# Performance work log

Hardware: AMD Instinct MI355X
Metric: run time of the kernel (lower is better)

Reference implementation:

```python
import jax, jax.numpy as jnp
from jax import lax
import numpy as np

B, T, K = 128, 256, 600


def setup_inputs() -> dict:
    key = jax.random.key(0)
    k1, k2, k3, k4 = jax.random.split(key, 4)
    potentials = jax.random.normal(k1, (B, T, K), dtype=jnp.float32)
    transitions = jax.random.normal(k2, (K, K), dtype=jnp.float32) * 0.1
    tags = jax.random.randint(k3, (B, T), 0, K, dtype=jnp.int32)
    seq_len = jax.random.randint(k4, (B,), T // 2, T + 1, dtype=jnp.int32)
    return {"potentials": potentials, "transitions": transitions,
            "tags": tags, "seq_len": seq_len}


def _sequence_score(potentials, transitions, tags, mask):
    # unary (emission) scores: sum_t potentials[b, t, tags[b, t]] over valid t
    emit = jnp.take_along_axis(potentials, tags[..., None], axis=-1)[..., 0]  # [B,T]
    unary = jnp.sum(emit * mask, axis=1)
    # binary (transition) scores for valid consecutive pairs
    trans = transitions[tags[:, :-1], tags[:, 1:]]  # [B,T-1]
    binary = jnp.sum(trans * mask[:, 1:], axis=1)
    return unary + binary


def _log_norm(potentials, transitions, mask):
    # forward algorithm over time via scan; alpha: [B,K]
    def step(alpha, inp):
        emit_t, mask_t = inp  # [B,K], [B]
        scores = alpha[:, :, None] + transitions[None]      # [B,K,K]
        new = jax.nn.logsumexp(scores, axis=1) + emit_t     # [B,K]
        alpha = jnp.where(mask_t[:, None], new, alpha)
        return alpha, None

    alpha0 = potentials[:, 0]
    xs = (jnp.swapaxes(potentials[:, 1:], 0, 1),
          jnp.swapaxes(mask[:, 1:] > 0, 0, 1))
    alpha, _ = lax.scan(step, alpha0, xs)
    return jax.nn.logsumexp(alpha, axis=-1)  # [B]


def _viterbi(potentials, transitions, mask):
    idk = jnp.arange(K, dtype=jnp.int32)

    def step(alpha, inp):
        emit_t, mask_t = inp
        scores = alpha[:, :, None] + transitions[None]   # [B,K,K]
        bp = jnp.argmax(scores, axis=1).astype(jnp.int32)  # [B,K]
        new = jnp.max(scores, axis=1) + emit_t
        alpha = jnp.where(mask_t[:, None], new, alpha)
        bp = jnp.where(mask_t[:, None], bp, idk[None, :])  # identity past seq end
        return alpha, bp

    alpha0 = potentials[:, 0]
    xs = (jnp.swapaxes(potentials[:, 1:], 0, 1),
          jnp.swapaxes(mask[:, 1:] > 0, 0, 1))
    alpha, bps = lax.scan(step, alpha0, xs)  # bps: [T-1,B,K]
    last = jnp.argmax(alpha, axis=-1).astype(jnp.int32)  # [B]

    def back(tag, bp):
        prev = jnp.take_along_axis(bp, tag[:, None], axis=1)[:, 0]
        return prev, prev

    _, prevs = lax.scan(back, last, bps, reverse=True)  # [T-1,B]
    seq = jnp.concatenate([prevs, last[None]], axis=0)  # [T,B]
    seq = jnp.swapaxes(seq, 0, 1)                       # [B,T]
    return seq * mask.astype(jnp.int32)


def reference(potentials, transitions, tags, seq_len):
    mask = (jnp.arange(T)[None, :] < seq_len[:, None]).astype(potentials.dtype)  # [B,T]
    score = _sequence_score(potentials, transitions, tags, mask)
    log_norm = _log_norm(potentials, transitions, mask)
    log_likelihood = score - log_norm            # [B]
    crf_loss = -jnp.mean(log_likelihood)         # scalar, as in train_step
    decode_sequence = _viterbi(potentials, transitions, mask)  # [B,T]
    return crf_loss, decode_sequence
```

## Files before the change

### kernel.cpp

```cpp
#include <hip/hip_runtime.h>
#include <stdint.h>

#define CRF_B 128
#define CRF_T 256
#define CRF_K 600
#define FWD_NT 640
#define NWAVE 10
#define QW 152
#define QG 96
#define QSTR (QW - QG)
#define ESC 60.0f
#define INV7620 (1.0f/7620.0f)

#if __has_builtin(__builtin_amdgcn_sdot4)
#define DOT4(a,b,c) __builtin_amdgcn_sdot4((int)(a),(int)(b),(int)(c),false)
#else
__device__ __forceinline__ int DOT4(uint32_t a, uint32_t b, int c) {
    c += (int)(int8_t)(a)       * (int)(int8_t)(b);
    c += (int)(int8_t)(a >> 8)  * (int)(int8_t)(b >> 8);
    c += (int)(int8_t)(a >> 16) * (int)(int8_t)(b >> 16);
    c += (int)(int8_t)(a >> 24) * (int)(int8_t)(b >> 24);
    return c;
}
#endif

__device__ __forceinline__ uint32_t fmono(float x) {
    uint32_t k = __float_as_uint(x);
    return (k & 0x80000000u) ? ~k : (k | 0x80000000u);
}
__device__ __forceinline__ float funmono(uint32_t k) {
    return __uint_as_float((k & 0x80000000u) ? (k ^ 0x80000000u) : ~k);
}

__global__ __launch_bounds__(256) void prepE_kernel(const float* __restrict__ trans,
                                                    uint32_t* __restrict__ EqT)
{
    int idx = blockIdx.x * 256 + threadIdx.x;
    if (idx < QW * CRF_K) {
        int q = idx / CRF_K, j = idx % CRF_K;
        uint32_t w = 0;
        #pragma unroll
        for (int k = 0; k < 4; ++k) {
            int i = 4 * q + k;
            int b = 0;
            if (i < CRF_K) {
                b = __float2int_rn(ESC * __expf(trans[i * CRF_K + j]));
                b = min(127, max(0, b));
            }
            w |= ((uint32_t)(b & 0xff)) << (8 * k);
        }
        EqT[idx] = w;
    }
}

__global__ __launch_bounds__(64) void prep2_kernel(const float* __restrict__ trans,
                                                   float* __restrict__ rowmax,
                                                   float* __restrict__ rowmin)
{
    int r = blockIdx.x;
    int lane = threadIdx.x;
    float mx = -INFINITY, mn = INFINITY;
    for (int j = lane; j < CRF_K; j += 64) {
        float v = trans[r * CRF_K + j];
        mx = fmaxf(mx, v);
        mn = fminf(mn, v);
    }
    for (int o = 32; o; o >>= 1) {
        mx = fmaxf(mx, __shfl_down(mx, o));
        mn = fminf(mn, __shfl_down(mn, o));
    }
    if (lane == 0) { rowmax[r] = mx; rowmin[r] = mn; }
}

__global__ __launch_bounds__(64) void score_kernel(const float* __restrict__ pot,
                                                   const float* __restrict__ trans,
                                                   const int* __restrict__ tags,
                                                   const int* __restrict__ seq_len,
                                                   float* __restrict__ scoreArr)
{
    int b = blockIdx.x;
    int lane = threadIdx.x;
    int L = seq_len[b];
    float s = 0.f;
    for (int t = lane; t < CRF_T; t += 64) {
        if (t < L) {
            int tg = tags[b * CRF_T + t];
            s += pot[((size_t)b * CRF_T + t) * CRF_K + tg];
            if (t >= 1) {
                int tp = tags[b * CRF_T + t - 1];
                s += trans[tp * CRF_K + tg];
            }
        }
    }
    for (int o = 32; o; o >>= 1) s += __shfl_down(s, o);
    if (lane == 0) scoreArr[b] = s;
}

__global__ __launch_bounds__(FWD_NT, 2) void fwd_kernel(
    const float* __restrict__ pot,
    const float* __restrict__ trans,
    const uint32_t* __restrict__ EqT,
    const float* __restrict__ rowmax,
    const float* __restrict__ rowmin,
    const int* __restrict__ seq_len,
    uint16_t* __restrict__ bp,
    float* __restrict__ lognormArr,
    int* __restrict__ lastArr)
{
    extern __shared__ uint32_t eLds[];
    const int bid = blockIdx.x;
    const int tid = threadIdx.x;
    const int lane = tid & 63, wid = tid >> 6;
    const bool act = tid < CRF_K;

    __shared__ __align__(16) float sAv[2][CRF_K];
    __shared__ int sCand[FWD_NT];
    __shared__ int sRedI[NWAVE];
    __shared__ __align__(16) uint32_t sAq[2][2][QW];
    __shared__ float sRedA[NWAVE], sRedB[NWAVE];
    __shared__ unsigned vSlot[2];
    __shared__ unsigned lSlot[2][2];
    __shared__ float sB0f, sB1f;
    __shared__ int sRedC[NWAVE];

    if (bid < CRF_B) {
        const int b = bid;
        const int L = seq_len[b];
        const float* pb = pot + (size_t)b * CRF_T * CRF_K;
        float rmx = act ? rowmax[tid] : 0.f;
        float rmn = act ? rowmin[tid] : 0.f;
        if (act) sAv[0][tid] = pb[tid];
        if (tid == 0) { vSlot[0] = 0u; vSlot[1] = 0u; }
        int cur = 0;
        __syncthreads();

        for (int t = 1; t < L; ++t) {
            float a_own = act ? sAv[cur][tid] : -INFINITY;
            float li = act ? a_own + rmn : -INFINITY;
            for (int o = 32; o; o >>= 1) li = fmaxf(li, __shfl_down(li, o));
            if (lane == 0) atomicMax(&vSlot[t & 1], fmono(li));
            __syncthreads();
            const float LB = funmono(vSlot[t & 1]);
            if (tid == 0) vSlot[(t + 1) & 1] = 0u;
            bool flag = act && (a_own + rmx >= LB);
            uint64_t mask = __ballot(flag);
            if (flag) sCand[(wid << 6) + __popcll(mask & ((1ull << lane) - 1ull))] = tid;
            if (lane == 0) sRedI[wid] = __popcll(mask);
            __syncthreads();
            float emitv = act ? pb[(size_t)t * CRF_K + tid] : 0.f;
            if (act) {
                float v = -INFINITY; int ix = 0;
                #pragma unroll 2
                for (int w = 0; w < NWAVE; ++w) {
                    const int cw = sRedI[w];
                    const int base = w << 6;
                    for (int k0 = 0; k0 < cw; k0 += 4) {
                        #pragma unroll
                        for (int u = 0; u < 4; ++u) {
                            int kk = k0 + u;
                            int i = sCand[base + ((kk < cw) ? kk : 0)];
                            float cnd = sAv[cur][i] + trans[i * CRF_K + tid];
                            if (cnd > v) { v = cnd; ix = i; }
                        }
                    }
                }
                bp[((size_t)b * (CRF_T - 1) + (t - 1)) * CRF_K + tid] = (uint16_t)ix;
                sAv[cur ^ 1][tid] = v + emitv;
            }
            cur ^= 1;
        }

        float mv = act ? sAv[cur][tid] : -INFINITY;
        float y = mv;
        for (int o = 32; o; o >>= 1) y = fmaxf(y, __shfl_down(y, o));
        if (lane == 0) sRedA[wid] = y;
        __syncthreads();
        if (tid == 0) { float m = sRedA[0]; for (int w = 1; w < NWAVE; ++w) m = fmaxf(m, sRedA[w]); sB0f = m; }
        __syncthreads();
        float vmax = sB0f;
        int cand = (act && mv == vmax) ? tid : 0x7fffffff;
        for (int o = 32; o; o >>= 1) cand = min(cand, __shfl_down(cand, o));
        if (lane == 0) sRedC[wid] = cand;
        __syncthreads();
        if (tid == 0) {
            int mi = sRedC[0];
            for (int w = 1; w < NWAVE; ++w) mi = min(mi, sRedC[w]);
            lastArr[b] = mi;
        }
    } else {
        const int q = bid - CRF_B;
        const int b0 = 2 * q, b1 = b0 + 1;
        const int L0 = seq_len[b0], L1 = seq_len[b1];
        const int Tmax = max(L0, L1);
        const float* pb0 = pot + (size_t)b0 * CRF_T * CRF_K;
        const float* pb1 = pot + (size_t)b1 * CRF_T * CRF_K;

        for (int w = tid; w < QSTR * CRF_K; w += FWD_NT)
            eLds[w] = EqT[QG * CRF_K + w];

        float p00 = act ? pb0[tid] : -INFINITY;
        float p01 = act ? pb1[tid] : -INFINITY;
        {
            float y0 = p00, y1 = p01;
            for (int o = 32; o; o >>= 1) { y0 = fmaxf(y0, __shfl_down(y0, o)); y1 = fmaxf(y1, __shfl_down(y1, o)); }
            if (lane == 0) { sRedA[wid] = y0; sRedB[wid] = y1; }
            __syncthreads();
            if (tid == 0) {
                float m0 = sRedA[0], m1 = sRedB[0];
                for (int w = 1; w < NWAVE; ++w) { m0 = fmaxf(m0, sRedA[w]); m1 = fmaxf(m1, sRedB[w]); }
                sB0f = m0; sB1f = m1;
            }
            __syncthreads();
        }
        float ls0 = sB0f, ls1 = sB1f;
        float lsf0 = ls0, lsf1 = ls1;
        float afin0 = 0.f, afin1 = 0.f;
        if (act) {
            float na0 = __expf(p00 - sB0f);
            float na1 = __expf(p01 - sB1f);
            uint8_t* d0 = (uint8_t*)&sAq[0][0][0];
            uint8_t* d1 = (uint8_t*)&sAq[0][1][0];
            d0[tid] = (uint8_t)__float2int_rn(127.0f * na0);
            d1[tid] = (uint8_t)__float2int_rn(127.0f * na1);
        }
        if (tid < 8) {
            ((uint8_t*)&sAq[0][0][150])[tid & 7] = 0;
            ((uint8_t*)&sAq[0][1][150])[tid & 7] = 0;
        }
        if (tid >= 632) {
            ((uint8_t*)&sAq[1][0][150])[tid - 632] = 0;
            ((uint8_t*)&sAq[1][1][150])[tid - 632] = 0;
        }
        if (tid == 0) { lSlot[0][0] = 0u; lSlot[0][1] = 0u; lSlot[1][0] = 0u; lSlot[1][1] = 0u; }
        int cur = 0;
        __syncthreads();

        for (int t = 1; t < Tmax; ++t) {
            const bool lv0 = t < L0, lv1 = t < L1;
            float na0v = 0.f, na1v = 0.f;
            if (act) {
                int Sa0 = 0, Sb0 = 0, Sa1 = 0, Sb1 = 0;
                const uint32_t* eg = EqT + tid;
                #pragma unroll 6
                for (int c = 0; c < QG / 4; ++c) {
                    uint32_t e0 = eg[(4 * c + 0) * CRF_K];
                    uint32_t e1 = eg[(4 * c + 1) * CRF_K];
                    uint32_t e2 = eg[(4 * c + 2) * CRF_K];
                    uint32_t e3 = eg[(4 * c + 3) * CRF_K];
                    uint4 a0 = *(const uint4*)&sAq[cur][0][4 * c];
                    uint4 a1 = *(const uint4*)&sAq[cur][1][4 * c];
                    Sa0 = DOT4(a0.x, e0, Sa0); Sb0 = DOT4(a0.y, e1, Sb0);
                    Sa0 = DOT4(a0.z, e2, Sa0); Sb0 = DOT4(a0.w, e3, Sb0);
                    Sa1 = DOT4(a1.x, e0, Sa1); Sb1 = DOT4(a1.y, e1, Sb1);
                    Sa1 = DOT4(a1.z, e2, Sa1); Sb1 = DOT4(a1.w, e3, Sb1);
                }
                const uint32_t* ecl = eLds + tid;
                #pragma unroll
                for (int s = 0; s < QSTR / 4; ++s) {
                    uint32_t e0 = ecl[(4 * s + 0) * CRF_K];
                    uint32_t e1 = ecl[(4 * s + 1) * CRF_K];
                    uint32_t e2 = ecl[(4 * s + 2) * CRF_K];
                    uint32_t e3 = ecl[(4 * s + 3) * CRF_K];
                    uint4 a0 = *(const uint4*)&sAq[cur][0][QG + 4 * s];
                    uint4 a1 = *(const uint4*)&sAq[cur][1][QG + 4 * s];
                    Sa0 = DOT4(a0.x, e0, Sa0); Sb0 = DOT4(a0.y, e1, Sb0);
                    Sa0 = DOT4(a0.z, e2, Sa0); Sb0 = DOT4(a0.w, e3, Sb0);
                    Sa1 = DOT4(a1.x, e0, Sa1); Sb1 = DOT4(a1.y, e1, Sb1);
                    Sa1 = DOT4(a1.z, e2, Sa1); Sb1 = DOT4(a1.w, e3, Sb1);
                }
                int S0 = Sa0 + Sb0, S1 = Sa1 + Sb1;
                if (lv0) na0v = (float)S0 * INV7620 * __expf(pb0[(size_t)t * CRF_K + tid]);
                if (lv1) na1v = (float)S1 * INV7620 * __expf(pb1[(size_t)t * CRF_K + tid]);
                if (t == L0 - 1) { afin0 = na0v; lsf0 = ls0; }
                if (t == L1 - 1) { afin1 = na1v; lsf1 = ls1; }
            }
            float m0r = na0v, m1r = na1v;
            for (int o = 32; o; o >>= 1) { m0r = fmaxf(m0r, __shfl_down(m0r, o)); m1r = fmaxf(m1r, __shfl_down(m1r, o)); }
            if (lane == 0) {
                atomicMax(&lSlot[0][t & 1], __float_as_uint(m0r));
                atomicMax(&lSlot[1][t & 1], __float_as_uint(m1r));
            }
            __syncthreads();
            float m0 = __uint_as_float(lSlot[0][t & 1]);
            float m1 = __uint_as_float(lSlot[1][t & 1]);
            if (tid == 0) { lSlot[0][(t + 1) & 1] = 0u; lSlot[1][(t + 1) & 1] = 0u; }
            if (act) {
                uint8_t* d0 = (uint8_t*)&sAq[cur ^ 1][0][0];
                uint8_t* d1 = (uint8_t*)&sAq[cur ^ 1][1][0];
                const uint8_t* s0 = (const uint8_t*)&sAq[cur][0][0];
                const uint8_t* s1 = (const uint8_t*)&sAq[cur][1][0];
                if (lv0) { ls0 += __logf(m0); d0[tid] = (uint8_t)__float2int_rn(na0v * (127.0f / m0)); }
                else     { d0[tid] = s0[tid]; }
                if (lv1) { ls1 += __logf(m1); d1[tid] = (uint8_t)__float2int_rn(na1v * (127.0f / m1)); }
                else     { d1[tid] = s1[tid]; }
            }
            __syncthreads();
            cur ^= 1;
        }

        float a0s = afin0, a1s = afin1;
        for (int o = 32; o; o >>= 1) { a0s += __shfl_down(a0s, o); a1s += __shfl_down(a1s, o); }
        if (lane == 0) { sRedA[wid] = a0s; sRedB[wid] = a1s; }
        __syncthreads();
        if (tid == 0) {
            float S0 = 0.f, S1 = 0.f;
            for (int w = 0; w < NWAVE; ++w) { S0 += sRedA[w]; S1 += sRedB[w]; }
            lognormArr[b0] = lsf0 + __logf(S0);
            lognormArr[b1] = lsf1 + __logf(S1);
        }
    }
}

__global__ __launch_bounds__(64) void backtrace_kernel(const uint16_t* __restrict__ bp,
                                                       const int* __restrict__ seq_len,
                                                       const int* __restrict__ lastArr,
                                                       float* __restrict__ out)
{
    int r = blockIdx.x * 64 + threadIdx.x;
    if (r >= CRF_B) return;
    int L = seq_len[r];
    float* o = out + 1 + (size_t)r * CRF_T;
    int tag = lastArr[r];
    for (int t = CRF_T - 1; t >= L; --t) o[t] = 0.f;
    o[L - 1] = (float)tag;
    for (int t = L - 2; t >= 0; --t) {
        tag = bp[((size_t)r * (CRF_T - 1) + t) * CRF_K + tag];
        o[t] = (float)tag;
    }
}

__global__ __launch_bounds__(128) void loss_kernel(const float* __restrict__ scoreArr,
                                                   const float* __restrict__ lognormArr,
                                                   float* __restrict__ out)
{
    int tid = threadIdx.x;
    float x = scoreArr[tid] - lognormArr[tid];
    for (int o = 32; o; o >>= 1) x += __shfl_down(x, o);
    __shared__ float r2[2];
    if ((tid & 63) == 0) r2[tid >> 6] = x;
    __syncthreads();
    if (tid == 0) out[0] = -(r2[0] + r2[1]) / (float)CRF_B;
}

extern "C" void kernel_launch(void* const* d_in, const int* in_sizes, int n_in,
                              void* d_out, int out_size, void* d_ws, size_t ws_size,
                              hipStream_t stream)
{
    const float* pot     = (const float*)d_in[0];
    const float* trans   = (const float*)d_in[1];
    const int*   tags    = (const int*)d_in[2];
    const int*   seq_len = (const int*)d_in[3];
    float* out = (float*)d_out;

    char* ws = (char*)d_ws;
    const size_t bpBytes  = (size_t)CRF_B * (CRF_T - 1) * CRF_K * 2;
    const size_t eqBytes  = (size_t)QW * CRF_K * 4;
    uint16_t* bp     = (uint16_t*)ws;
    uint32_t* EqT    = (uint32_t*)(ws + bpBytes);
    float*    rowmax = (float*)(ws + bpBytes + eqBytes);
    float*    rowmin = rowmax + CRF_K;
    float* scoreArr   = rowmin + CRF_K;
    float* lognormArr = scoreArr + CRF_B;
    int*   lastArr    = (int*)(lognormArr + CRF_B);

    prepE_kernel<<<(QW * CRF_K + 255) / 256, 256, 0, stream>>>(trans, EqT);
    prep2_kernel<<<CRF_K, 64, 0, stream>>>(trans, rowmax, rowmin);
    score_kernel<<<CRF_B, 64, 0, stream>>>(pot, trans, tags, seq_len, scoreArr);
    fwd_kernel<<<CRF_B + CRF_B / 2, FWD_NT, QSTR * CRF_K * 4, stream>>>(
        pot, trans, EqT, rowmax, rowmin, seq_len, bp, lognormArr, lastArr);
    backtrace_kernel<<<(CRF_B + 63) / 64, 64, 0, stream>>>(bp, seq_len, lastArr, out);
    loss_kernel<<<1, 128, 0, stream>>>(scoreArr, lognormArr, out);
}
```

Measured before the change: 1.919 ms.

## Give each forward-algorithm block one sequence with 4 columns per thread

The log-normalizer blocks now each handle a single sequence instead of a pair, so the grid grows from 192 to 256 blocks. Each of 150 active threads computes four output columns using vectorized uint4 loads of the int8 transition matrix and packs four quantized alphas into one word. The global/LDS split of the transition rows moves slightly (QG 96 to 92). The aim is to stop a short sequence from waiting on its longer partner's step count and to cut per-column load instructions. The cost is that only 150 of 640 threads do dot-product work and there are more blocks contending for the GPU.

```diff
diff --git a/kernel.cpp b/kernel.cpp
--- a/kernel.cpp
+++ b/kernel.cpp
@@ -7,7 +7,7 @@
 #define FWD_NT 640
 #define NWAVE 10
 #define QW 152
-#define QG 96
+#define QG 92
 #define QSTR (QW - QG)
 #define ESC 60.0f
 #define INV7620 (1.0f/7620.0f)
@@ -96,6 +96,17 @@
     if (lane == 0) scoreArr[b] = s;
 }
 
+#define CHUNK(APTR, EPTR, CH) { \
+    uint4 a  = *(const uint4*)((APTR) + 4 * (CH)); \
+    uint4 e0 = *(const uint4*)((EPTR) + (size_t)(4 * (CH) + 0) * CRF_K); \
+    uint4 e1 = *(const uint4*)((EPTR) + (size_t)(4 * (CH) + 1) * CRF_K); \
+    uint4 e2 = *(const uint4*)((EPTR) + (size_t)(4 * (CH) + 2) * CRF_K); \
+    uint4 e3 = *(const uint4*)((EPTR) + (size_t)(4 * (CH) + 3) * CRF_K); \
+    S0 = DOT4(a.x, e0.x, S0); S1 = DOT4(a.x, e0.y, S1); S2 = DOT4(a.x, e0.z, S2); S3 = DOT4(a.x, e0.w, S3); \
+    S0 = DOT4(a.y, e1.x, S0); S1 = DOT4(a.y, e1.y, S1); S2 = DOT4(a.y, e1.z, S2); S3 = DOT4(a.y, e1.w, S3); \
+    S0 = DOT4(a.z, e2.x, S0); S1 = DOT4(a.z, e2.y, S1); S2 = DOT4(a.z, e2.z, S2); S3 = DOT4(a.z, e2.w, S3); \
+    S0 = DOT4(a.w, e3.x, S0); S1 = DOT4(a.w, e3.y, S1); S2 = DOT4(a.w, e3.z, S2); S3 = DOT4(a.w, e3.w, S3); }
+
 __global__ __launch_bounds__(FWD_NT, 2) void fwd_kernel(
     const float* __restrict__ pot,
     const float* __restrict__ trans,
@@ -116,11 +127,11 @@
     __shared__ __align__(16) float sAv[2][CRF_K];
     __shared__ int sCand[FWD_NT];
     __shared__ int sRedI[NWAVE];
-    __shared__ __align__(16) uint32_t sAq[2][2][QW];
-    __shared__ float sRedA[NWAVE], sRedB[NWAVE];
+    __shared__ __align__(16) uint32_t sAq[2][QW];
+    __shared__ float sRedA[NWAVE];
     __shared__ unsigned vSlot[2];
-    __shared__ unsigned lSlot[2][2];
-    __shared__ float sB0f, sB1f;
+    __shared__ unsigned lSlot[2];
+    __shared__ float sB0f;
     __shared__ int sRedC[NWAVE];
 
     if (bid < CRF_B) {
@@ -188,125 +199,89 @@
             lastArr[b] = mi;
         }
     } else {
-        const int q = bid - CRF_B;
-        const int b0 = 2 * q, b1 = b0 + 1;
-        const int L0 = seq_len[b0], L1 = seq_len[b1];
-        const int Tmax = max(L0, L1);
-        const float* pb0 = pot + (size_t)b0 * CRF_T * CRF_K;
-        const float* pb1 = pot + (size_t)b1 * CRF_T * CRF_K;
+        const int b = bid - CRF_B;
+        const int L = seq_len[b];
+        const float* pb = pot + (size_t)b * CRF_T * CRF_K;
+        const bool cact = tid < CRF_K / 4;
+        const int j0 = 4 * tid;
 
         for (int w = tid; w < QSTR * CRF_K; w += FWD_NT)
-            eLds[w] = EqT[QG * CRF_K + w];
-
-        float p00 = act ? pb0[tid] : -INFINITY;
-        float p01 = act ? pb1[tid] : -INFINITY;
+            eLds[w] = EqT[(size_t)QG * CRF_K + w];
+
+        float4 p0 = cact ? *(const float4*)(pb + j0)
+                         : make_float4(-INFINITY, -INFINITY, -INFINITY, -INFINITY);
         {
-            float y0 = p00, y1 = p01;
-            for (int o = 32; o; o >>= 1) { y0 = fmaxf(y0, __shfl_down(y0, o)); y1 = fmaxf(y1, __shfl_down(y1, o)); }
-            if (lane == 0) { sRedA[wid] = y0; sRedB[wid] = y1; }
-            __syncthreads();
-            if (tid == 0) {
-                float m0 = sRedA[0], m1 = sRedB[0];
-                for (int w = 1; w < NWAVE; ++w) { m0 = fmaxf(m0, sRedA[w]); m1 = fmaxf(m1, sRedB[w]); }
-                sB0f = m0; sB1f = m1;
-            }
-            __syncthreads();
-        }
-        float ls0 = sB0f, ls1 = sB1f;
-        float lsf0 = ls0, lsf1 = ls1;
-        float afin0 = 0.f, afin1 = 0.f;
-        if (act) {
-            float na0 = __expf(p00 - sB0f);
-            float na1 = __expf(p01 - sB1f);
-            uint8_t* d0 = (uint8_t*)&sAq[0][0][0];
-            uint8_t* d1 = (uint8_t*)&sAq[0][1][0];
-            d0[tid] = (uint8_t)__float2int_rn(127.0f * na0);
-            d1[tid] = (uint8_t)__float2int_rn(127.0f * na1);
-        }
-        if (tid < 8) {
-            ((uint8_t*)&sAq[0][0][150])[tid & 7] = 0;
-            ((uint8_t*)&sAq[0][1][150])[tid & 7] = 0;
-        }
-        if (tid >= 632) {
-            ((uint8_t*)&sAq[1][0][150])[tid - 632] = 0;
-            ((uint8_t*)&sAq[1][1][150])[tid - 632] = 0;
-        }
-        if (tid == 0) { lSlot[0][0] = 0u; lSlot[0][1] = 0u; lSlot[1][0] = 0u; lSlot[1][1] = 0u; }
+            float y = fmaxf(fmaxf(p0.x, p0.y), fmaxf(p0.z, p0.w));
+            for (int o = 32; o; o >>= 1) y = fmaxf(y, __shfl_down(y, o));
+            if (lane == 0) sRedA[wid] = y;
+            __syncthreads();
+            if (tid == 0) { float m = sRedA[0]; for (int w = 1; w < NWAVE; ++w) m = fmaxf(m, sRedA[w]); sB0f = m; }
+            __syncthreads();
+        }
+        float m0 = sB0f;
+        float ls = m0, lsf = m0;
+        float afin = 0.f;
+        if (cact) {
+            uint32_t w = 0;
+            w |= (uint32_t)(__float2int_rn(127.0f * __expf(p0.x - m0)) & 0xff);
+            w |= (uint32_t)(__float2int_rn(127.0f * __expf(p0.y - m0)) & 0xff) << 8;
+            w |= (uint32_t)(__float2int_rn(127.0f * __expf(p0.z - m0)) & 0xff) << 16;
+            w |= (uint32_t)(__float2int_rn(127.0f * __expf(p0.w - m0)) & 0xff) << 24;
+            sAq[0][tid] = w;
+        }
+        if (tid >= 636) {
+            sAq[0][150 + (tid & 1)] = 0u;
+            sAq[1][150 + (tid & 1)] = 0u;
+        }
+        if (tid == 0) { lSlot[0] = 0u; lSlot[1] = 0u; }
         int cur = 0;
         __syncthreads();
 
-        for (int t = 1; t < Tmax; ++t) {
-            const bool lv0 = t < L0, lv1 = t < L1;
-            float na0v = 0.f, na1v = 0.f;
-            if (act) {
-                int Sa0 = 0, Sb0 = 0, Sa1 = 0, Sb1 = 0;
-                const uint32_t* eg = EqT + tid;
-                #pragma unroll 6
-                for (int c = 0; c < QG / 4; ++c) {
-                    uint32_t e0 = eg[(4 * c + 0) * CRF_K];
-                    uint32_t e1 = eg[(4 * c + 1) * CRF_K];
-                    uint32_t e2 = eg[(4 * c + 2) * CRF_K];
-                    uint32_t e3 = eg[(4 * c + 3) * CRF_K];
-                    uint4 a0 = *(const uint4*)&sAq[cur][0][4 * c];
-                    uint4 a1 = *(const uint4*)&sAq[cur][1][4 * c];
-                    Sa0 = DOT4(a0.x, e0, Sa0); Sb0 = DOT4(a0.y, e1, Sb0);
-                    Sa0 = DOT4(a0.z, e2, Sa0); Sb0 = DOT4(a0.w, e3, Sb0);
-                    Sa1 = DOT4(a1.x, e0, Sa1); Sb1 = DOT4(a1.y, e1, Sb1);
-                    Sa1 = DOT4(a1.z, e2, Sa1); Sb1 = DOT4(a1.w, e3, Sb1);
-                }
-                const uint32_t* ecl = eLds + tid;
-                #pragma unroll
-                for (int s = 0; s < QSTR / 4; ++s) {
-                    uint32_t e0 = ecl[(4 * s + 0) * CRF_K];
-                    uint32_t e1 = ecl[(4 * s + 1) * CRF_K];
-                    uint32_t e2 = ecl[(4 * s + 2) * CRF_K];
-                    uint32_t e3 = ecl[(4 * s + 3) * CRF_K];
-                    uint4 a0 = *(const uint4*)&sAq[cur][0][QG + 4 * s];
-                    uint4 a1 = *(const uint4*)&sAq[cur][1][QG + 4 * s];
-                    Sa0 = DOT4(a0.x, e0, Sa0); Sb0 = DOT4(a0.y, e1, Sb0);
-                    Sa0 = DOT4(a0.z, e2, Sa0); Sb0 = DOT4(a0.w, e3, Sb0);
-                    Sa1 = DOT4(a1.x, e0, Sa1); Sb1 = DOT4(a1.y, e1, Sb1);
-                    Sa1 = DOT4(a1.z, e2, Sa1); Sb1 = DOT4(a1.w, e3, Sb1);
-                }
-                int S0 = Sa0 + Sb0, S1 = Sa1 + Sb1;
-                if (lv0) na0v = (float)S0 * INV7620 * __expf(pb0[(size_t)t * CRF_K + tid]);
-                if (lv1) na1v = (float)S1 * INV7620 * __expf(pb1[(size_t)t * CRF_K + tid]);
-                if (t == L0 - 1) { afin0 = na0v; lsf0 = ls0; }
-                if (t == L1 - 1) { afin1 = na1v; lsf1 = ls1; }
-            }
-            float m0r = na0v, m1r = na1v;
-            for (int o = 32; o; o >>= 1) { m0r = fmaxf(m0r, __shfl_down(m0r, o)); m1r = fmaxf(m1r, __shfl_down(m1r, o)); }
-            if (lane == 0) {
-                atomicMax(&lSlot[0][t & 1], __float_as_uint(m0r));
-                atomicMax(&lSlot[1][t & 1], __float_as_uint(m1r));
-            }
-            __syncthreads();
-            float m0 = __uint_as_float(lSlot[0][t & 1]);
-            float m1 = __uint_as_float(lSlot[1][t & 1]);
-            if (tid == 0) { lSlot[0][(t + 1) & 1] = 0u; lSlot[1][(t + 1) & 1] = 0u; }
-            if (act) {
-                uint8_t* d0 = (uint8_t*)&sAq[cur ^ 1][0][0];
-                uint8_t* d1 = (uint8_t*)&sAq[cur ^ 1][1][0];
-                const uint8_t* s0 = (const uint8_t*)&sAq[cur][0][0];
-                const uint8_t* s1 = (const uint8_t*)&sAq[cur][1][0];
-                if (lv0) { ls0 += __logf(m0); d0[tid] = (uint8_t)__float2int_rn(na0v * (127.0f / m0)); }
-                else     { d0[tid] = s0[tid]; }
-                if (lv1) { ls1 += __logf(m1); d1[tid] = (uint8_t)__float2int_rn(na1v * (127.0f / m1)); }
-                else     { d1[tid] = s1[tid]; }
+        for (int t = 1; t < L; ++t) {
+            float na0 = 0.f, na1 = 0.f, na2 = 0.f, na3 = 0.f;
+            if (cact) {
+                int S0 = 0, S1 = 0, S2 = 0, S3 = 0;
+                const uint32_t* eg = EqT + j0;
+                #pragma unroll 4
+                for (int ch = 0; ch < QG / 4; ++ch) CHUNK(&sAq[cur][0], eg, ch)
+                const uint32_t* el = eLds + j0;
+                #pragma unroll 4
+                for (int ch = 0; ch < QSTR / 4; ++ch) CHUNK(&sAq[cur][QG], el, ch)
+                float4 em = *(const float4*)(pb + (size_t)t * CRF_K + j0);
+                na0 = (float)S0 * INV7620 * __expf(em.x);
+                na1 = (float)S1 * INV7620 * __expf(em.y);
+                na2 = (float)S2 * INV7620 * __expf(em.z);
+                na3 = (float)S3 * INV7620 * __expf(em.w);
+            }
+            float mx = fmaxf(fmaxf(na0, na1), fmaxf(na2, na3));
+            for (int o = 32; o; o >>= 1) mx = fmaxf(mx, __shfl_down(mx, o));
+            if (lane == 0) atomicMax(&lSlot[t & 1], __float_as_uint(mx));
+            __syncthreads();
+            float m = __uint_as_float(lSlot[t & 1]);
+            if (tid == 0) lSlot[(t + 1) & 1] = 0u;
+            if (t == L - 1) { afin = na0 + na1 + na2 + na3; lsf = ls; }
+            ls += __logf(m);
+            if (cact) {
+                float s = 127.0f / m;
+                uint32_t w = 0;
+                w |= (uint32_t)(__float2int_rn(na0 * s) & 0xff);
+                w |= (uint32_t)(__float2int_rn(na1 * s) & 0xff) << 8;
+                w |= (uint32_t)(__float2int_rn(na2 * s) & 0xff) << 16;
+                w |= (uint32_t)(__float2int_rn(na3 * s) & 0xff) << 24;
+                sAq[cur ^ 1][tid] = w;
             }
             __syncthreads();
             cur ^= 1;
         }
 
-        float a0s = afin0, a1s = afin1;
-        for (int o = 32; o; o >>= 1) { a0s += __shfl_down(a0s, o); a1s += __shfl_down(a1s, o); }
-        if (lane == 0) { sRedA[wid] = a0s; sRedB[wid] = a1s; }
+        float a0s = afin;
+        for (int o = 32; o; o >>= 1) a0s += __shfl_down(a0s, o);
+        if (lane == 0) sRedA[wid] = a0s;
         __syncthreads();
         if (tid == 0) {
-            float S0 = 0.f, S1 = 0.f;
-            for (int w = 0; w < NWAVE; ++w) { S0 += sRedA[w]; S1 += sRedB[w]; }
-            lognormArr[b0] = lsf0 + __logf(S0);
-            lognormArr[b1] = lsf1 + __logf(S1);
+            float S = 0.f;
+            for (int w = 0; w < NWAVE; ++w) S += sRedA[w];
+            lognormArr[b] = lsf + __logf(S);
         }
     }
 }
@@ -366,7 +341,7 @@
     prepE_kernel<<<(QW * CRF_K + 255) / 256, 256, 0, stream>>>(trans, EqT);
     prep2_kernel<<<CRF_K, 64, 0, stream>>>(trans, rowmax, rowmin);
     score_kernel<<<CRF_B, 64, 0, stream>>>(pot, trans, tags, seq_len, scoreArr);
-    fwd_kernel<<<CRF_B + CRF_B / 2, FWD_NT, QSTR * CRF_K * 4, stream>>>(
+    fwd_kernel<<<2 * CRF_B, FWD_NT, QSTR * CRF_K * 4, stream>>>(
         pot, trans, EqT, rowmax, rowmin, seq_len, bp, lognormArr, lastArr);
     backtrace_kernel<<<(CRF_B + 63) / 64, 64, 0, stream>>>(bp, seq_len, lastArr, out);
     loss_kernel<<<1, 128, 0, stream>>>(scoreArr, lognormArr, out);
```

Result: slower. 1.982 ms (+3.3%).
